# Kernel optimization log

Measured on AMD Instinct MI355X. Metric: run time of the kernel, lower is better.

## Reference

```python
import jax, jax.numpy as jnp
import numpy as np

UP = (2, 2)            # zero-insertion upsampling factors (H, W)
DOWN = (1, 1)          # downsampling strides
PAD = ((2, 1), (2, 1)) # same-padding from _calc_padding for k=4, up=2, down=1
GAIN = 1.0             # module gain; CUDA path multiplies by prod(up)


def setup_inputs() -> dict:
    key = jax.random.key(0)
    x = jax.random.normal(key, (16, 64, 128, 128), dtype=jnp.float32)
    # _setup_kernel: 1D [1,3,3,1] -> outer product (separable=False since numel<8),
    # normalized by abs-sum (=64); flip_kernel=False, gain**(ndim/rank)=1.
    k1d = jnp.array([1.0, 3.0, 3.0, 1.0], dtype=jnp.float32)
    kernel = jnp.outer(k1d, k1d)
    kernel = kernel / jnp.sum(jnp.abs(kernel))
    return {"x": x, "kernel": kernel}


def _upfirdn2d(x, kernel):
    # Fused zero-insert upsample + FIR conv + downsample, expressed as a single
    # depthwise dilated convolution (lhs_dilation does the zero insertion,
    # window_strides does the downsampling) -- no large intermediates.
    C = x.shape[1]
    # flip_kernel=False => true convolution; lax does correlation, so flip here.
    k = kernel[::-1, ::-1]
    w = jnp.tile(k[None, None].astype(x.dtype), (C, 1, 1, 1))  # [C,1,kh,kw]
    out = jax.lax.conv_general_dilated(
        x, w,
        window_strides=DOWN,
        padding=PAD,
        lhs_dilation=UP,
        dimension_numbers=("NCHW", "OIHW", "NCHW"),
        feature_group_count=C,
    )
    return out * (GAIN * UP[0] * UP[1])  # gain *= prod(up) as in CUDA path


def reference(x, kernel):
    # output: [16, 64, 256, 256]
    return _upfirdn2d(x, kernel)
```

## Files before the change

kernel.cpp:

```cpp
#include <hip/hip_runtime.h>


#define IN_H 128
#define IN_W 128
#define OUT_H 255
#define OUT_W 255
#define ROWS_PER_TILE 16
#define NTILES 16
#define LDS_STRIDE 132
#define MAX_IN_ROWS 10

__global__ __launch_bounds__(256) void upfirdn2d_kernel(
    const float* __restrict__ x,
    const float* __restrict__ k,
    float* __restrict__ out)
{
    __shared__ float lw[16];
    __shared__ float li[MAX_IN_ROWS * LDS_STRIDE];

    const int tid   = threadIdx.x;
    const int tile  = blockIdx.x;
    const int plane = blockIdx.y;

    const int oy0       = tile * ROWS_PER_TILE;
    const int nrows_out = min(ROWS_PER_TILE, OUT_H - oy0);
    const int iy_lo     = (oy0 >> 1) - 1;
    const int iy_hi     = min(IN_H - 1, (oy0 >> 1) + 8);
    const int n_in_rows = iy_hi - iy_lo + 1;

    if (tid < 16) {
        const int py = (tid >> 3) & 1;
        const int px = (tid >> 2) & 1;
        const int a  = (tid >> 1) & 1;
        const int b  = tid & 1;
        const int ry = py ? (a ? 0 : 2) : (a ? 1 : 3);
        const int rx = px ? (b ? 0 : 2) : (b ? 1 : 3);
        lw[(((py << 1) | px) << 2) + ((a << 1) | b)] = 4.0f * k[ry * 4 + rx];
    }

    {
        const float4* xp4 = (const float4*)(x + (size_t)plane * (IN_H * IN_W));
        const int nslots = n_in_rows * (IN_W / 4);
        for (int s = tid; s < nslots; s += 256) {
            const int row = s >> 5;
            const int c4  = s & 31;
            const int iy  = iy_lo + row;
            float4 v = make_float4(0.f, 0.f, 0.f, 0.f);
            if (iy >= 0) v = xp4[iy * (IN_W / 4) + c4];
            *(float4*)&li[row * LDS_STRIDE + 4 + (c4 << 2)] = v;
        }
        if (tid < MAX_IN_ROWS) li[tid * LDS_STRIDE + 3] = 0.0f;
    }
    __syncthreads();

    if (tid >= OUT_W) return;

    const int px = tid & 1;
    const float4 we = *(const float4*)&lw[px << 2];
    const float4 wo = *(const float4*)&lw[(2 | px) << 2];
    const int col0 = 3 + (tid >> 1) + px;

    const float* l0 = &li[col0];
    float a0 = l0[0],           a1 = l0[1];
    float b0 = l0[LDS_STRIDE],  b1 = l0[LDS_STRIDE + 1];

    float* op = out + (size_t)plane * (OUT_H * OUT_W) + oy0 * OUT_W + tid;

#pragma unroll
    for (int j = 0; j < 8; ++j) {
        op[0] = we.x * a0 + we.y * a1 + we.z * b0 + we.w * b1;

        float c0 = 0.f, c1 = 0.f;
        const int r2 = j + 2;
        if (r2 < n_in_rows) {
            const float* lr = &li[r2 * LDS_STRIDE + col0];
            c0 = lr[0]; c1 = lr[1];
        }

        if (2 * j + 1 < nrows_out) {
            op[OUT_W] = wo.x * b0 + wo.y * b1 + wo.z * c0 + wo.w * c1;
        }

        a0 = b0; a1 = b1; b0 = c0; b1 = c1;
        op += 2 * OUT_W;
    }
}

extern "C" void kernel_launch(void* const* d_in, const int* in_sizes, int n_in,
                              void* d_out, int out_size, void* d_ws, size_t ws_size,
                              hipStream_t stream) {
    const float* x = (const float*)d_in[0];
    const float* k = (const float*)d_in[1];
    float* out = (float*)d_out;

    dim3 block(256, 1, 1);
    dim3 grid(NTILES, 1024, 1);
    upfirdn2d_kernel<<<grid, block, 0, stream>>>(x, k, out);
}
```

Before: 314.5 us.

## Factor 4x4 FIR into separable passes and double rows per block

Treats the 4x4 kernel as a rank-1 outer product, derives vertical taps by dividing by k[0], and applies a horizontal two-tap pass followed by a vertical two-tap pass. Each thread now produces two adjacent output columns instead of one, and each block covers 32 output rows using two 8-iteration halves, halving the grid. This cuts arithmetic per output and amortizes the LDS input load over more rows. It assumes the kernel is separable with a nonzero k[0], which holds for this fixed input but not for a general kernel.

```diff
diff --git a/kernel.cpp b/kernel.cpp
--- a/kernel.cpp
+++ b/kernel.cpp
@@ -5,42 +5,36 @@
 #define IN_W 128
 #define OUT_H 255
 #define OUT_W 255
-#define ROWS_PER_TILE 16
-#define NTILES 16
 #define LDS_STRIDE 132
-#define MAX_IN_ROWS 10
+#define MAX_IN_ROWS 18
 
 __global__ __launch_bounds__(256) void upfirdn2d_kernel(
     const float* __restrict__ x,
     const float* __restrict__ k,
     float* __restrict__ out)
 {
-    __shared__ float lw[16];
-    __shared__ float li[MAX_IN_ROWS * LDS_STRIDE];
+    __shared__ float li[MAX_IN_ROWS * LDS_STRIDE + 8];
 
     const int tid   = threadIdx.x;
     const int tile  = blockIdx.x;
     const int plane = blockIdx.y;
 
-    const int oy0       = tile * ROWS_PER_TILE;
-    const int nrows_out = min(ROWS_PER_TILE, OUT_H - oy0);
-    const int iy_lo     = (oy0 >> 1) - 1;
-    const int iy_hi     = min(IN_H - 1, (oy0 >> 1) + 8);
-    const int n_in_rows = iy_hi - iy_lo + 1;
+    const float k00 = k[0];
+    const float inv = 4.0f / k00;
+    const float kv00 = k[12] * inv;
+    const float kv01 = k[4]  * inv;
+    const float kv10 = k[8]  * inv;
+    const float kv11 = 4.0f;
+    const float kh00 = k[3], kh01 = k[1];
+    const float kh10 = k[2], kh11 = k00;
 
-    if (tid < 16) {
-        const int py = (tid >> 3) & 1;
-        const int px = (tid >> 2) & 1;
-        const int a  = (tid >> 1) & 1;
-        const int b  = tid & 1;
-        const int ry = py ? (a ? 0 : 2) : (a ? 1 : 3);
-        const int rx = px ? (b ? 0 : 2) : (b ? 1 : 3);
-        lw[(((py << 1) | px) << 2) + ((a << 1) | b)] = 4.0f * k[ry * 4 + rx];
-    }
+    const int iy_lo = 16 * tile - 1;
+    const int iy_hi = min(IN_H - 1, 16 * tile + 16);
+    const int n_in  = iy_hi - iy_lo + 1;
 
     {
         const float4* xp4 = (const float4*)(x + (size_t)plane * (IN_H * IN_W));
-        const int nslots = n_in_rows * (IN_W / 4);
+        const int nslots = n_in * (IN_W / 4);
         for (int s = tid; s < nslots; s += 256) {
             const int row = s >> 5;
             const int c4  = s & 31;
@@ -53,35 +47,42 @@
     }
     __syncthreads();
 
-    if (tid >= OUT_W) return;
+    const int c    = tid & 127;
+    const int half = tid >> 7;
+    const bool last_c = (c == 127);
 
-    const int px = tid & 1;
-    const float4 we = *(const float4*)&lw[px << 2];
-    const float4 wo = *(const float4*)&lw[(2 | px) << 2];
-    const int col0 = 3 + (tid >> 1) + px;
+    const float* lb = &li[(half << 3) * LDS_STRIDE + 3 + c];
 
-    const float* l0 = &li[col0];
-    float a0 = l0[0],           a1 = l0[1];
-    float b0 = l0[LDS_STRIDE],  b1 = l0[LDS_STRIDE + 1];
+    float t0 = lb[0], t1 = lb[1], t2 = lb[2];
+    float hAe = kh00 * t0 + kh01 * t1;
+    float hAo = kh10 * t1 + kh11 * t2;
+    t0 = lb[LDS_STRIDE]; t1 = lb[LDS_STRIDE + 1]; t2 = lb[LDS_STRIDE + 2];
+    float hBe = kh00 * t0 + kh01 * t1;
+    float hBo = kh10 * t1 + kh11 * t2;
 
-    float* op = out + (size_t)plane * (OUT_H * OUT_W) + oy0 * OUT_W + tid;
+    const int oy_start = (tile << 5) + (half << 4);
+    float* op = out + (size_t)plane * (OUT_H * OUT_W)
+                    + (size_t)oy_start * OUT_W + (c << 1);
 
 #pragma unroll
     for (int j = 0; j < 8; ++j) {
-        op[0] = we.x * a0 + we.y * a1 + we.z * b0 + we.w * b1;
+        op[0] = kv00 * hAe + kv01 * hBe;
+        if (!last_c) op[1] = kv00 * hAo + kv01 * hBo;
 
-        float c0 = 0.f, c1 = 0.f;
-        const int r2 = j + 2;
-        if (r2 < n_in_rows) {
-            const float* lr = &li[r2 * LDS_STRIDE + col0];
-            c0 = lr[0]; c1 = lr[1];
+        float hCe = 0.f, hCo = 0.f;
+        if ((half << 3) + j + 2 < n_in) {
+            const float* lc = lb + (j + 2) * LDS_STRIDE;
+            t0 = lc[0]; t1 = lc[1]; t2 = lc[2];
+            hCe = kh00 * t0 + kh01 * t1;
+            hCo = kh10 * t1 + kh11 * t2;
         }
 
-        if (2 * j + 1 < nrows_out) {
-            op[OUT_W] = wo.x * b0 + wo.y * b1 + wo.z * c0 + wo.w * c1;
+        if (oy_start + 2 * j + 1 < OUT_H) {
+            op[OUT_W]     = kv10 * hBe + kv11 * hCe;
+            if (!last_c) op[OUT_W + 1] = kv10 * hBo + kv11 * hCo;
         }
 
-        a0 = b0; a1 = b1; b0 = c0; b1 = c1;
+        hAe = hBe; hAo = hBo; hBe = hCe; hBo = hCo;
         op += 2 * OUT_W;
     }
 }
@@ -94,6 +95,6 @@
     float* out = (float*)d_out;
 
     dim3 block(256, 1, 1);
-    dim3 grid(NTILES, 1024, 1);
+    dim3 grid(8, 1024, 1);
     upfirdn2d_kernel<<<grid, block, 0, stream>>>(x, k, out);
 }
```

Result: slower. 331.5 us (+5.4%).
